# Performance work log

Hardware: AMD Instinct MI355X
Metric: run time of the kernel (lower is better)

The kernel has to match this reference:

```python
import jax, jax.numpy as jnp
import numpy as np

L = 20        # num layers (TTS LM)
Q = 512       # query length
PAST = 512    # past_kv_len
END = PAST + Q  # end_step = 1024
MAXS = 2048   # max_seq_len
D = 896       # hidden size
NKV = 2       # KV heads
NQ = 14       # Q heads
G = NQ // NKV # GQA repeat = 7
HD = 64       # head dim
FF = 4864     # SwiGLU intermediate (Qwen2.5-0.5B)
EPS = 1e-6
SCALE = 1.0 / np.sqrt(HD)


def rms_norm(x, w):
    return x * jax.lax.rsqrt(jnp.mean(x * x, axis=-1, keepdims=True) + EPS) * w


def rotate_half(x):
    x1, x2 = jnp.split(x, 2, axis=-1)
    return jnp.concatenate([-x2, x1], axis=-1)


def setup_inputs() -> dict:
    key = jax.random.key(0)
    ks = jax.random.split(key, 24)
    s = 0.02
    inp = {
        'hidden_states': jax.random.normal(ks[0], (1, Q, D), jnp.float32),
        'position_cos': jax.random.uniform(ks[1], (1, Q, HD), jnp.float32, -1.0, 1.0),
        'position_sin': jax.random.uniform(ks[2], (1, Q, HD), jnp.float32, -1.0, 1.0),
        'attention_mask': jnp.zeros((1, 1, Q, END), jnp.float32),
        'inject_mode': jnp.zeros((1,), jnp.float32),
        'inject_k': jax.random.normal(ks[3], (1, L * NKV, Q, HD), jnp.float32),
        'inject_v': jax.random.normal(ks[4], (1, L * NKV, Q, HD), jnp.float32),
        'k_cache': (jax.random.normal(ks[5], (L, 1, NKV, MAXS, HD), jnp.float32) * 0.5).astype(jnp.float16),
        'v_cache': (jax.random.normal(ks[6], (L, 1, NKV, MAXS, HD), jnp.float32) * 0.5).astype(jnp.float16),
        'Wq': jax.random.normal(ks[7], (L, D, NQ * HD), jnp.float32) * s,
        'bq': jax.random.normal(ks[8], (L, NQ * HD), jnp.float32) * s,
        'Wk': jax.random.normal(ks[9], (L, D, NKV * HD), jnp.float32) * s,
        'bk': jax.random.normal(ks[10], (L, NKV * HD), jnp.float32) * s,
        'Wv': jax.random.normal(ks[11], (L, D, NKV * HD), jnp.float32) * s,
        'bv': jax.random.normal(ks[12], (L, NKV * HD), jnp.float32) * s,
        'Wo': jax.random.normal(ks[13], (L, NQ * HD, D), jnp.float32) * s,
        'ln1': jnp.ones((L, D), jnp.float32),
        'ln2': jnp.ones((L, D), jnp.float32),
        'Wg': jax.random.normal(ks[14], (L, D, FF), jnp.float32) * s,
        'Wu': jax.random.normal(ks[15], (L, D, FF), jnp.float32) * s,
        'Wd': jax.random.normal(ks[16], (L, FF, D), jnp.float32) * s,
        'final_w': jnp.ones((D,), jnp.float32),
    }
    return inp


def reference(hidden_states, position_cos, position_sin, attention_mask,
              inject_mode, inject_k, inject_v, k_cache, v_cache,
              Wq, bq, Wk, bk, Wv, bv, Wo, ln1, ln2, Wg, Wu, Wd, final_w):
    cos = position_cos[:, None]   # [1,1,Q,HD]
    sin = position_sin[:, None]
    inj = inject_mode[0]
    normal = 1.0 - inj
    mask = attention_mask[:, None]  # [1,1,1,Q,END] broadcast over (g,h)
    # per-layer inject slices: [L,1,NKV,Q,HD]
    ik = jnp.transpose(inject_k.reshape(1, L, NKV, Q, HD), (1, 0, 2, 3, 4))
    iv = jnp.transpose(inject_v.reshape(1, L, NKV, Q, HD), (1, 0, 2, 3, 4))

    def layer_fn(h, p):
        (wq, bq_, wk, bk_, wv, bv_, wo, l1, l2, wg, wu, wd, kc, vc, ikl, ivl) = p
        residual = h
        x = rms_norm(h, l1)
        q = (x @ wq + bq_).reshape(1, Q, NQ, HD).transpose(0, 2, 1, 3)   # [1,NQ,Q,HD]
        k = (x @ wk + bk_).reshape(1, Q, NKV, HD).transpose(0, 2, 1, 3)  # [1,NKV,Q,HD]
        v = (x @ wv + bv_).reshape(1, Q, NKV, HD).transpose(0, 2, 1, 3)
        q = q * cos + rotate_half(q) * sin
        k = k * cos + rotate_half(k) * sin
        k = normal * k + inj * ikl
        v = normal * v + inj * ivl
        kc = kc.at[:, :, PAST:END].set(k.astype(jnp.float16))
        vc = vc.at[:, :, PAST:END].set(v.astype(jnp.float16))
        kf = kc[:, :, :END].astype(jnp.float32)  # [1,NKV,END,HD]
        vf = vc[:, :, :END].astype(jnp.float32)
        qg = q.reshape(1, NKV, G, Q, HD)         # grouped GQA (== repeat_kv)
        scores = jnp.einsum('bghqd,bgkd->bghqk', qg, kf) * SCALE + mask
        w = jax.nn.softmax(scores, axis=-1)
        o = jnp.einsum('bghqk,bgkd->bghqd', w, vf)
        o = o.reshape(1, NQ, Q, HD).transpose(0, 2, 1, 3).reshape(1, Q, NQ * HD)
        h = residual + o @ wo
        residual = h
        x = rms_norm(h, l2)
        h = residual + (jax.nn.silu(x @ wg) * (x @ wu)) @ wd
        return h, None

    xs = (Wq, bq, Wk, bk, Wv, bv, Wo, ln1, ln2, Wg, Wu, Wd, k_cache, v_cache, ik, iv)
    h, _ = jax.lax.scan(layer_fn, hidden_states, xs)
    return rms_norm(h, final_w)
```

## Files before the change

kernel.cpp:

```cpp
#include <hip/hip_runtime.h>
#include <hip/hip_fp16.h>
#include <hip/hip_cooperative_groups.h>

namespace cg = cooperative_groups;

#define NLAYER 20
#define QLEN 512
#define PAST 512
#define ENDS 1024
#define MAXS 2048
#define DMODEL 896
#define NKV 2
#define NQ 14
#define GQ 7
#define HD 64
#define FF 4864
#define RMSEPS 1e-6f
#define ATT_SCALE 0.125f

typedef _Float16 f16x8 __attribute__((ext_vector_type(8)));
typedef float f32x4 __attribute__((ext_vector_type(4)));
typedef unsigned int u32_;

__device__ __forceinline__ void gld16(const void* g, void* l) {
    __builtin_amdgcn_global_load_lds(
        (const __attribute__((address_space(1))) u32_*)g,
        (__attribute__((address_space(3))) u32_*)l, 16, 0, 0);
}

union SmemU {
    struct { __half As[8192]; __half Bs[8192]; } g;
    struct { __half S[16512]; float rowinv[16]; } a;
    struct { float T[32][129]; } p;
    struct { float red[4]; } r;
};

#define GEMM_STAGE_SETUP(A_, lda_, B_, ldb_, Kps_)                              \
    const int lane = t & 63, wave = t >> 6;                                     \
    const int wm = wave >> 1, wn = wave & 1;                                    \
    const int m0 = by * 128, n0 = bx * 128;                                     \
    const int kb0 = bz * (Kps_);                                                \
    const int sr = t >> 2, sc = (t & 3) * 8;                                    \
    const int la = lane & 15, ka = (lane >> 4) * 8;                             \
    const int nIter = (Kps_) >> 5;                                              \
    const int scw = sc ^ (((sr >> 1) & 3) << 3);                                \
    const size_t a0 = (size_t)(m0 + sr) * (lda_) + kb0 + scw;                   \
    const size_t a1 = (size_t)(m0 + sr + 64) * (lda_) + kb0 + scw;              \
    const size_t b0 = (size_t)(n0 + sr) * (ldb_) + kb0 + scw;                   \
    const size_t b1 = (size_t)(n0 + sr + 64) * (ldb_) + kb0 + scw;              \
    const int l0 = sr * 32 + sc, l1 = (sr + 64) * 32 + sc;                      \
    f32x4 acc[4][4] = {};                                                       \
    gld16(&(A_)[a0], &As[l0]);                                                  \
    gld16(&(A_)[a1], &As[l1]);                                                  \
    gld16(&(B_)[b0], &Bs[l0]);                                                  \
    gld16(&(B_)[b1], &Bs[l1]);                                                  \
    int buf = 0;                                                                \
    for (int kt = 0; kt < nIter; kt++) {                                        \
        __syncthreads();                                                        \
        if (kt + 1 < nIter) {                                                   \
            const int ko = (kt + 1) * 32;                                       \
            gld16(&(A_)[a0 + ko], &As[(buf ^ 1) * 4096 + l0]);                  \
            gld16(&(A_)[a1 + ko], &As[(buf ^ 1) * 4096 + l1]);                  \
            gld16(&(B_)[b0 + ko], &Bs[(buf ^ 1) * 4096 + l0]);                  \
            gld16(&(B_)[b1 + ko], &Bs[(buf ^ 1) * 4096 + l1]);                  \
        }                                                                       \
        f16x8 av[4], bv[4];                                                     \
        _Pragma("unroll")                                                       \
        for (int i = 0; i < 4; i++) {                                           \
            const int row = wm * 64 + i * 16 + la;                              \
            av[i] = *(const f16x8*)&As[buf * 4096 + row * 32 + (ka ^ (((row >> 1) & 3) << 3))]; \
        }                                                                       \
        _Pragma("unroll")                                                       \
        for (int j = 0; j < 4; j++) {                                           \
            const int row = wn * 64 + j * 16 + la;                              \
            bv[j] = *(const f16x8*)&Bs[buf * 4096 + row * 32 + (ka ^ (((row >> 1) & 3) << 3))]; \
        }                                                                       \
        _Pragma("unroll")                                                       \
        for (int i = 0; i < 4; i++)                                             \
            _Pragma("unroll")                                                   \
            for (int j = 0; j < 4; j++)                                         \
                acc[i][j] = __builtin_amdgcn_mfma_f32_16x16x32_f16(av[i], bv[j], acc[i][j], 0, 0, 0); \
        buf ^= 1;                                                               \
    }                                                                           \
    __syncthreads();

__device__ __forceinline__ void gemm_body(
    const __half* __restrict__ A, int lda, const __half* __restrict__ B, int ldb,
    float* __restrict__ outP, __half* __restrict__ actP, int N, int Kps, int mode,
    int bx, int by, int bz, int t, __half* As, __half* Bs)
{
    GEMM_STAGE_SETUP(A, lda, B, ldb, Kps)
    const int r0 = m0 + wm * 64 + (lane >> 4) * 4;
    const int c0 = n0 + wn * 64 + la;
    if (mode == 0) {
        float* o = outP + (size_t)bz * QLEN * N;
#pragma unroll
        for (int i = 0; i < 4; i++)
#pragma unroll
            for (int j = 0; j < 4; j++)
#pragma unroll
                for (int r = 0; r < 4; r++)
                    o[(size_t)(r0 + i * 16 + r) * N + c0 + j * 16] = acc[i][j][r];
    } else {
#pragma unroll
        for (int i = 0; i < 4; i++)
#pragma unroll
            for (int j = 0; j < 4; j++)
#pragma unroll
                for (int r = 0; r < 4; r++) {
                    float v = acc[i][j][r];
                    float other = __shfl_xor(v, 1);
                    if (!(la & 1)) {
                        const int c = c0 + j * 16;
                        const int row = r0 + i * 16 + r;
                        float sg = v / (1.f + __expf(-v));
                        actP[(size_t)row * FF + (c >> 1)] = __float2half(sg * other);
                    }
                }
    }
}

__device__ __forceinline__ void gemm_qkv_body(
    const __half* __restrict__ A, const __half* __restrict__ B,
    const float* __restrict__ bqkv, const float* __restrict__ cosb,
    const float* __restrict__ sinb, float inj,
    const float* __restrict__ injk, const float* __restrict__ injv,
    __half* __restrict__ qr, __half* __restrict__ Ka, __half* __restrict__ Vt,
    int layer, int bx, int by, int t, __half* As, __half* Bs)
{
    const int bz = 0;
    GEMM_STAGE_SETUP(A, DMODEL, B, DMODEL, 896)
    const int r0 = m0 + wm * 64 + (lane >> 4) * 4;
    const int c0 = n0 + wn * 64 + la;
    const float nrm = 1.f - inj;
#pragma unroll
    for (int i = 0; i < 4; i++)
#pragma unroll
        for (int j = 0; j < 4; j++)
#pragma unroll
            for (int r = 0; r < 4; r++) {
                const int pn = r0 + i * 16 + r;
                const int c = c0 + j * 16;
                const int d = c & 63;
                float v = acc[i][j][r] + bqkv[c];
                if (c < 1024) {
                    float pvv = acc[i][j ^ 2][r] + bqkv[c ^ 32];
                    float rot = (d < 32) ? -pvv : pvv;
                    float rv = v * cosb[pn * HD + d] + rot * sinb[pn * HD + d];
                    if (c < 896) {
                        qr[((size_t)(c >> 6) * QLEN + pn) * HD + d] = __float2half(rv);
                    } else {
                        const int kvh = (c - 896) >> 6;
                        float kn = nrm * rv + inj * injk[(((size_t)layer * NKV + kvh) * QLEN + pn) * HD + d];
                        Ka[((size_t)kvh * ENDS + PAST + pn) * HD + d] = __float2half(kn);
                    }
                } else {
                    const int kvh = (c - 1024) >> 6;
                    float vn = nrm * v + inj * injv[(((size_t)layer * NKV + kvh) * QLEN + pn) * HD + d];
                    Vt[((size_t)kvh * HD + d) * ENDS + PAST + pn] = __float2half(vn);
                }
            }
}

__device__ __forceinline__ void prep_body(
    const float* __restrict__ Wq, const float* __restrict__ Wk, const float* __restrict__ Wv,
    const float* __restrict__ Wo, const float* __restrict__ Wg, const float* __restrict__ Wu,
    const float* __restrict__ Wd, int layer, int z, int bx, int t, float (*T)[129],
    __half* __restrict__ dstW)
{
    const int K = (z == 3) ? FF : DMODEL;
    const int N = (z == 0) ? 1152 : (z == 2) ? 2 * FF : DMODEL;
    const int tilesN = N / 128;
    const int tk = bx / tilesN, tn = bx % tilesN;
    const int k0 = tk * 32, n0 = tn * 128;
    const float* src; int ldn, nc0; int isU = 0;
    if (z == 0) {
        if (n0 < 896)        { src = Wq + (size_t)layer * 896 * 896; ldn = 896; nc0 = n0; }
        else if (n0 < 1024)  { src = Wk + (size_t)layer * 896 * 128; ldn = 128; nc0 = n0 - 896; }
        else                 { src = Wv + (size_t)layer * 896 * 128; ldn = 128; nc0 = n0 - 1024; }
    } else if (z == 1) { src = Wo + (size_t)layer * 896 * 896; ldn = 896; nc0 = n0; }
    else if (z == 2) {
        if (n0 < FF) { src = Wg + (size_t)layer * 896 * FF; ldn = FF; nc0 = n0; }
        else         { src = Wu + (size_t)layer * 896 * FF; ldn = FF; nc0 = n0 - FF; isU = 1; }
    } else { src = Wd + (size_t)layer * FF * 896; ldn = 896; nc0 = n0; }

    __syncthreads();
    {
        const int r = t >> 3, cb = (t & 7) * 16;
        const float* s = &src[(size_t)(k0 + r) * ldn + nc0 + cb];
#pragma unroll
        for (int q = 0; q < 4; q++) {
            float4 v = *(const float4*)&s[q * 4];
            T[r][cb + q * 4 + 0] = v.x; T[r][cb + q * 4 + 1] = v.y;
            T[r][cb + q * 4 + 2] = v.z; T[r][cb + q * 4 + 3] = v.w;
        }
    }
    __syncthreads();
    {
        const int nr = t >> 1, kh = (t & 1) * 16;
        const int drow = (z == 2) ? (2 * (nc0 + nr) + isU) : (n0 + nr);
        __half tmp[16];
#pragma unroll
        for (int kk = 0; kk < 16; kk++)
            tmp[kk] = __float2half_rn(T[kh + kk][nr]);
        __half* dst = dstW + (size_t)drow * K + k0 + kh;
        *(uint4*)dst = *(const uint4*)&tmp[0];
        *(uint4*)(dst + 8) = *(const uint4*)&tmp[8];
    }
    __syncthreads();
}

__device__ __forceinline__ void prep_dispatch(
    const float* Wq, const float* Wk, const float* Wv, const float* Wo,
    const float* Wg, const float* Wu, const float* Wd,
    const float* bq, const float* bk, const float* bv,
    int layer, int j, int t, float (*T)[129],
    __half* wq, __half* wo, __half* wgu, __half* wd, float* bqkv)
{
    int z; __half* dst; int bx = j;
    if (j < 252)        { z = 0; dst = wq; }
    else if (j < 448)   { z = 1; dst = wo;  bx -= 252; }
    else if (j < 2576)  { z = 2; dst = wgu; bx -= 448; }
    else                { z = 3; dst = wd;  bx -= 2576; }
    prep_body(Wq, Wk, Wv, Wo, Wg, Wu, Wd, layer, z, bx, t, T, dst);
    if (z == 0 && bx == 0) {
        for (int i = t; i < 1152; i += 256) {
            float b = (i < 896) ? bq[(size_t)layer * 896 + i]
                    : (i < 1024) ? bk[(size_t)layer * 128 + i - 896]
                                 : bv[(size_t)layer * 128 + i - 1024];
            bqkv[i] = b;
        }
    }
}

__device__ __forceinline__ void cache_copy_body(
    const float* __restrict__ kc32, const float* __restrict__ vc32, int layer,
    __half* __restrict__ Ka, __half* __restrict__ Vt, int p, int lt)
{
    const int kvh = lt >> 6, d = lt & 63;
    const size_t idx = (((size_t)layer * NKV + kvh) * MAXS + p) * HD + d;
    Ka[((size_t)kvh * ENDS + p) * HD + d] = __float2half(kc32[idx]);
    Vt[((size_t)kvh * HD + d) * ENDS + p] = __float2half(vc32[idx]);
}

__device__ __forceinline__ void ropekv_body(
    const float* __restrict__ part, const float* __restrict__ bias,
    const float* __restrict__ cosb, const float* __restrict__ sinb,
    const float* __restrict__ injm, const float* __restrict__ injk,
    const float* __restrict__ injv, const float* __restrict__ kc32,
    const float* __restrict__ vc32, int layer, int nsplit,
    __half* __restrict__ qr, __half* __restrict__ Ka, __half* __restrict__ Vt,
    int p, int lt)
{
    const int kvh = lt >> 6, d = lt & 63;
    if (p < PAST) { cache_copy_body(kc32, vc32, layer, Ka, Vt, p, lt); return; }
    const int pn = p - PAST;
    const float inj = injm[0], nrm = 1.f - inj;
    const float* rb = part + (size_t)pn * 1152;
    const size_t sst = (size_t)QLEN * 1152;
    auto rsum = [&](int c) {
        float x = bias[c];
        for (int s = 0; s < nsplit; s++) x += rb[(size_t)s * sst + c];
        return x;
    };
    for (int idx = lt; idx < NQ * HD; idx += 128) {
        const int dd = idx & 63;
        float x = rsum(idx);
        int pc = (dd < 32) ? idx + 32 : idx - 32;
        float pv = rsum(pc);
        if (dd < 32) pv = -pv;
        float rv = x * cosb[pn * HD + dd] + pv * sinb[pn * HD + dd];
        qr[((size_t)(idx >> 6) * QLEN + pn) * HD + dd] = __float2half(rv);
    }
    {
        const int c = NQ * HD + lt;
        float x = rsum(c);
        int pc = (d < 32) ? c + 32 : c - 32;
        float pv = rsum(pc);
        if (d < 32) pv = -pv;
        float rv = x * cosb[pn * HD + d] + pv * sinb[pn * HD + d];
        float kn = nrm * rv + inj * injk[(((size_t)layer * NKV + kvh) * QLEN + pn) * HD + d];
        Ka[((size_t)kvh * ENDS + PAST + pn) * HD + d] = __float2half(kn);
        const int cv = NQ * HD + NKV * HD + lt;
        float vv = rsum(cv);
        float vn = nrm * vv + inj * injv[(((size_t)layer * NKV + kvh) * QLEN + pn) * HD + d];
        Vt[((size_t)kvh * HD + d) * ENDS + PAST + pn] = __float2half(vn);
    }
}

__device__ __forceinline__ int sswz(int row, int col) {
    return row * 1032 + (col ^ ((row & 7) << 3));
}

__device__ __forceinline__ void attn_body(
    const __half* __restrict__ qr, const __half* __restrict__ Ka,
    const __half* __restrict__ Vt, const float* __restrict__ mask,
    __half* __restrict__ ob, int q0, int h, int t, __half* S, float* rowinv)
{
    const int kv = h / GQ;
    const int lane = t & 63, w = t >> 6;
    const int la = lane & 15, kg = lane >> 4;

    const f16x8* qp = (const f16x8*)&qr[((size_t)h * QLEN + q0 + la) * HD + kg * 8];
    const f16x8 qa0 = qp[0], qa1 = qp[4];
    __syncthreads();

    for (int kb = 0; kb < 256; kb += 16) {
        const int key = w * 256 + kb + la;
        const f16x8* kp = (const f16x8*)&Ka[((size_t)kv * ENDS + key) * HD + kg * 8];
        f32x4 s4 = {0.f, 0.f, 0.f, 0.f};
        s4 = __builtin_amdgcn_mfma_f32_16x16x32_f16(qa0, kp[0], s4, 0, 0, 0);
        s4 = __builtin_amdgcn_mfma_f32_16x16x32_f16(qa1, kp[4], s4, 0, 0, 0);
#pragma unroll
        for (int r = 0; r < 4; r++) {
            const int row = kg * 4 + r;
            float sv = s4[r] * ATT_SCALE + mask[(size_t)(q0 + row) * ENDS + key];
            S[sswz(row, key)] = __float2half(sv);
        }
    }
    __syncthreads();
    {
        const int row = w * 4 + kg;
        float mx = -1e30f;
        for (int j = 0; j < 64; j++)
            mx = fmaxf(mx, __half2float(S[sswz(row, la + 16 * j)]));
        for (int o = 1; o < 16; o <<= 1) mx = fmaxf(mx, __shfl_xor(mx, o));
        float sum = 0.f;
        for (int j = 0; j < 64; j++) {
            const int idx = sswz(row, la + 16 * j);
            float e = __expf(__half2float(S[idx]) - mx);
            S[idx] = __float2half(e);
            sum += e;
        }
        for (int o = 1; o < 16; o <<= 1) sum += __shfl_xor(sum, o);
        if (la == 0) rowinv[row] = 1.f / sum;
    }
    __syncthreads();
    {
        const int d = 16 * w + la;
        const __half* vrow = &Vt[((size_t)kv * HD + d) * ENDS];
        f32x4 acc = {0.f, 0.f, 0.f, 0.f};
        for (int ks = 0; ks < ENDS; ks += 32) {
            f16x8 pa = *(const f16x8*)&S[sswz(la, ks + kg * 8)];
            f16x8 vb = *(const f16x8*)&vrow[ks + kg * 8];
            acc = __builtin_amdgcn_mfma_f32_16x16x32_f16(pa, vb, acc, 0, 0, 0);
        }
#pragma unroll
        for (int r = 0; r < 4; r++) {
            const int qrow = kg * 4 + r;
            ob[(size_t)(q0 + qrow) * (NQ * HD) + h * HD + d] =
                __float2half(acc[r] * rowinv[qrow]);
        }
    }
    __syncthreads();
}

__device__ inline void cvt_store(float* p, float v)  { *p = v; }
__device__ inline void cvt_store(__half* p, float v) { *p = __float2half(v); }

template <typename OUT>
__device__ __forceinline__ void rms_body(
    float* __restrict__ h, const float* __restrict__ parts, int nparts,
    const float* __restrict__ w, OUT* __restrict__ out, int m, int t,
    float* red, float scale)
{
    float loc[4];
    float ss = 0.f;
    int r = 0;
    for (int i = t; i < DMODEL; i += 256, r++) {
        float x = h[(size_t)m * DMODEL + i];
        for (int s = 0; s < nparts; s++)
            x += parts[(size_t)s * QLEN * DMODEL + (size_t)m * DMODEL + i];
        loc[r] = x;
        if (nparts) h[(size_t)m * DMODEL + i] = x;
        ss += x * x;
    }
    for (int o = 32; o; o >>= 1) ss += __shfl_xor(ss, o);
    if ((t & 63) == 0) red[t >> 6] = ss;
    __syncthreads();
    float rs = rsqrtf((red[0] + red[1] + red[2] + red[3]) / (float)DMODEL + RMSEPS);
    r = 0;
    for (int i = t; i < DMODEL; i += 256, r++)
        cvt_store(&out[(size_t)m * DMODEL + i], loc[r] * rs * w[i] * scale);
    __syncthreads();
}

struct P22 {
    const float *hidden, *cosb, *sinb, *mask, *injm, *injk, *injv, *kc32, *vc32;
    const float *Wq, *bq, *Wk, *bk, *Wv, *bv, *Wo, *ln1, *ln2, *Wg, *Wu, *Wd, *finw;
    float *h; __half *xn, *qr, *Ka, *Vt, *ob, *act; float *BIGR;
    float *bqkv0, *bqkv1;
    __half *wq0, *wo0, *wgu0, *wd0, *wq1, *wo1, *wgu1, *wd1;
    float *outF;
};

#define PC_A 300
#define PC_B 700
#define PC_C 576
#define PC_D 800
#define PC_E 500
#define PC_F 600
#define PC_G 164
#define PB_A 0
#define PB_B 300
#define PB_C 1000
#define PB_D 1576
#define PB_E 2376
#define PB_F 2876
#define PB_G 3476

__global__ __launch_bounds__(256) void mega_kernel(P22 P)
{
    __shared__ SmemU sm;
    cg::grid_group gg = cg::this_grid();
    const int nb = gridDim.x, bid = blockIdx.x, t = threadIdx.x;
    const float inj = P.injm[0];

    for (int j = bid; j < 1792; j += nb) {
        int i = j * 256 + t;
        if (i < QLEN * DMODEL) P.h[i] = P.hidden[i];
    }
    for (int j = bid; j < 3640; j += nb)
        prep_dispatch(P.Wq, P.Wk, P.Wv, P.Wo, P.Wg, P.Wu, P.Wd, P.bq, P.bk, P.bv,
                      0, j, t, sm.p.T, P.wq0, P.wo0, P.wgu0, P.wd0, P.bqkv0);
    gg.sync();

    for (int l = 0; l < NLAYER; l++) {
        const int pb = l & 1;
        const __half* wq  = pb ? P.wq1  : P.wq0;
        const __half* wo  = pb ? P.wo1  : P.wo0;
        const __half* wgu = pb ? P.wgu1 : P.wgu0;
        const __half* wd  = pb ? P.wd1  : P.wd0;
        const float*  bqk = pb ? P.bqkv1 : P.bqkv0;
        const bool hasN = (l + 1 < NLAYER);
        __half* nwq  = pb ? P.wq0  : P.wq1;
        __half* nwo  = pb ? P.wo0  : P.wo1;
        __half* nwgu = pb ? P.wgu0 : P.wgu1;
        __half* nwd  = pb ? P.wd0  : P.wd1;
        float*  nbq  = pb ? P.bqkv0 : P.bqkv1;
        #define PREPN(idx) prep_dispatch(P.Wq, P.Wk, P.Wv, P.Wo, P.Wg, P.Wu, P.Wd, \
            P.bq, P.bk, P.bv, l + 1, (idx), t, sm.p.T, nwq, nwo, nwgu, nwd, nbq)

        for (int j = bid; j < QLEN + (hasN ? PC_A : 0); j += nb) {
            if (j < QLEN)
                rms_body<__half>(P.h, l ? P.BIGR : nullptr, l ? 8 : 0,
                                 P.ln1 + (size_t)l * DMODEL, P.xn, j, t, sm.r.red, 1.f);
            else PREPN(PB_A + j - QLEN);
        }
        gg.sync();

        for (int j = bid; j < 292 + (hasN ? PC_B : 0); j += nb) {
            if (j < 36)
                gemm_qkv_body(P.xn, wq, bqk, P.cosb, P.sinb, inj, P.injk, P.injv,
                              P.qr, P.Ka, P.Vt, l, j % 9, j / 9, t, sm.g.As, sm.g.Bs);
            else if (j < 292) {
                int p = (j - 36) * 2 + (t >> 7);
                cache_copy_body(P.kc32, P.vc32, l, P.Ka, P.Vt, p, t & 127);
            } else PREPN(PB_B + j - 292);
        }
        gg.sync();

        for (int j = bid; j < 448 + (hasN ? PC_C : 0); j += nb) {
            if (j < 448)
                attn_body(P.qr, P.Ka, P.Vt, P.mask, P.ob, (j & 31) * 16, j >> 5, t,
                          sm.a.S, sm.a.rowinv);
            else PREPN(PB_C + j - 448);
        }
        gg.sync();

        for (int j = bid; j < 112 + (hasN ? PC_D : 0); j += nb) {
            if (j < 112) {
                int z = j / 28, r = j % 28;
                gemm_body(P.ob, DMODEL, wo, DMODEL, P.BIGR, nullptr, DMODEL, 224, 0,
                          r % 7, r / 7, z, t, sm.g.As, sm.g.Bs);
            } else PREPN(PB_D + j - 112);
        }
        gg.sync();

        for (int j = bid; j < QLEN + (hasN ? PC_E : 0); j += nb) {
            if (j < QLEN)
                rms_body<__half>(P.h, P.BIGR, 4, P.ln2 + (size_t)l * DMODEL, P.xn,
                                 j, t, sm.r.red, 1.f);
            else PREPN(PB_E + j - QLEN);
        }
        gg.sync();

        for (int j = bid; j < 304 + (hasN ? PC_F : 0); j += nb) {
            if (j < 304)
                gemm_body(P.xn, DMODEL, wgu, DMODEL, nullptr, P.act, 2 * FF, DMODEL, 1,
                          j % 76, j / 76, 0, t, sm.g.As, sm.g.Bs);
            else PREPN(PB_F + j - 304);
        }
        gg.sync();

        for (int j = bid; j < 224 + (hasN ? PC_G : 0); j += nb) {
            if (j < 224) {
                int z = j / 28, r = j % 28;
                gemm_body(P.act, FF, wd, FF, P.BIGR, nullptr, DMODEL, 608, 0,
                          r % 7, r / 7, z, t, sm.g.As, sm.g.Bs);
            } else PREPN(PB_G + j - 224);
        }
        gg.sync();
        #undef PREPN
    }
    for (int j = bid; j < QLEN; j += nb)
        rms_body<float>(P.h, P.BIGR, 8, P.finw, P.outF, j, t, sm.r.red, 1.f);
}

__global__ __launch_bounds__(256) void init_kernel(
    const float* __restrict__ hidden, float* __restrict__ h, int* __restrict__ flags)
{
    const int idx = blockIdx.x * 256 + threadIdx.x;
    if (blockIdx.x == 0 && threadIdx.x < 8) flags[threadIdx.x] = 0;
    if (idx < QLEN * DMODEL) h[idx] = hidden[idx];
}

__global__ __launch_bounds__(256) void prep_all(
    const float* Wq, const float* Wk, const float* Wv, const float* Wo,
    const float* Wg, const float* Wu, const float* Wd,
    const float* bq, const float* bk, const float* bv, int layer,
    __half* wqkv, __half* wo, __half* wgu, __half* wd, float* bqkv)
{
    __shared__ float T[32][129];
    prep_dispatch(Wq, Wk, Wv, Wo, Wg, Wu, Wd, bq, bk, bv, layer, blockIdx.x,
                  threadIdx.x, T, wqkv, wo, wgu, wd, bqkv);
}

__global__ __launch_bounds__(256) void gemm128(
    const __half* A, int lda, const __half* B, int ldb,
    float* outP, __half* actP, int N, int Kps, int mode)
{
    __shared__ SmemU sm;
    gemm_body(A, lda, B, ldb, outP, actP, N, Kps, mode,
              blockIdx.x, blockIdx.y, blockIdx.z, threadIdx.x, sm.g.As, sm.g.Bs);
}

__global__ __launch_bounds__(128) void ropekv_kernel(
    const float* part, const float* bias, const float* cosb, const float* sinb,
    const float* injm, const float* injk, const float* injv,
    const float* kc32, const float* vc32, int layer, int nsplit,
    __half* qr, __half* Ka, __half* Vt)
{
    ropekv_body(part, bias, cosb, sinb, injm, injk, injv, kc32, vc32,
                layer, nsplit, qr, Ka, Vt, blockIdx.x, threadIdx.x);
}

__global__ __launch_bounds__(256) void attn_mfma(
    const __half* qr, const __half* Ka, const __half* Vt, const float* mask, __half* ob)
{
    __shared__ SmemU sm;
    attn_body(qr, Ka, Vt, mask, ob, blockIdx.x * 16, blockIdx.y, threadIdx.x,
              sm.a.S, sm.a.rowinv);
}

template <typename OUT>
__global__ __launch_bounds__(256) void rms_kernel(
    float* h, const float* parts, int nparts, const float* w, OUT* out,
    const int* flags)
{
    __shared__ float red[4];
    rms_body<OUT>(h, parts, nparts, w, out, blockIdx.x, threadIdx.x, red, 1.f);
}

extern "C" void kernel_launch(void* const* d_in, const int* in_sizes, int n_in,
                              void* d_out, int out_size, void* d_ws, size_t ws_size,
                              hipStream_t stream)
{
    const float*  hidden = (const float*)d_in[0];
    const float*  cosb   = (const float*)d_in[1];
    const float*  sinb   = (const float*)d_in[2];
    const float*  mask   = (const float*)d_in[3];
    const float*  injm   = (const float*)d_in[4];
    const float*  injk   = (const float*)d_in[5];
    const float*  injv   = (const float*)d_in[6];
    const float*  kc32   = (const float*)d_in[7];
    const float*  vc32   = (const float*)d_in[8];
    const float*  Wq     = (const float*)d_in[9];
    const float*  bq     = (const float*)d_in[10];
    const float*  Wk     = (const float*)d_in[11];
    const float*  bk     = (const float*)d_in[12];
    const float*  Wv     = (const float*)d_in[13];
    const float*  bv     = (const float*)d_in[14];
    const float*  Wo     = (const float*)d_in[15];
    const float*  ln1    = (const float*)d_in[16];
    const float*  ln2    = (const float*)d_in[17];
    const float*  Wg     = (const float*)d_in[18];
    const float*  Wu     = (const float*)d_in[19];
    const float*  Wd     = (const float*)d_in[20];
    const float*  finw   = (const float*)d_in[21];

    bool size_ok = (n_in == 22) &&
        in_sizes[0] == 458752 && in_sizes[1] == 32768 && in_sizes[3] == 524288 &&
        in_sizes[4] == 1 && in_sizes[5] == 1310720 && in_sizes[7] == 5242880 &&
        in_sizes[9] == 16056320 && in_sizes[10] == 17920 && in_sizes[11] == 2293760 &&
        in_sizes[15] == 16056320 && in_sizes[16] == 17920 && in_sizes[18] == 87162880 &&
        in_sizes[20] == 87162880 && in_sizes[21] == 896;
    if (!size_ok) { hipMemsetAsync(d_out, 0x42, (size_t)out_size * 4, stream); return; }

    char* ws = (char*)d_ws;
    size_t off = 0;
    auto alloc = [&](size_t bytes) { void* p = ws + off; off += (bytes + 255) & ~255ull; return p; };
    int*    flags = (int*)alloc(256);
    float*  bqkv0 = (float*)alloc(1152 * 4);
    float*  bqkv1 = (float*)alloc(1152 * 4);
    float*  h     = (float*)alloc((size_t)QLEN * DMODEL * 4);
    __half* xn    = (__half*)alloc((size_t)QLEN * DMODEL * 2);
    __half* qr    = (__half*)alloc((size_t)NQ * QLEN * HD * 2);
    __half* Ka    = (__half*)alloc((size_t)NKV * ENDS * HD * 2);
    __half* Vt    = (__half*)alloc((size_t)NKV * ENDS * HD * 2);
    __half* ob    = (__half*)alloc((size_t)QLEN * NQ * HD * 2);
    __half* act   = (__half*)alloc((size_t)QLEN * FF * 2);
    float*  BIGR  = (float*)alloc(8ull * QLEN * 1152 * 4);
    __half* wq0   = (__half*)alloc(2064384);
    __half* wo0   = (__half*)alloc(1605632);
    __half* wgu0  = (__half*)alloc(17432576);
    __half* wd0   = (__half*)alloc(8716288);
    const size_t NEED_LEGACY = off;
    __half* wq1   = (__half*)alloc(2064384);
    __half* wo1   = (__half*)alloc(1605632);
    __half* wgu1  = (__half*)alloc(17432576);
    __half* wd1   = (__half*)alloc(8716288);
    const size_t NEED_MEGA = off;

    if (ws_size < NEED_LEGACY) {
        hipMemsetAsync(d_out, 0, (size_t)out_size * 4, stream);
        return;
    }

    bool mega_ok = (ws_size >= NEED_MEGA);
    if (mega_ok) {
        int maxB = 0;
        hipError_t e = hipOccupancyMaxActiveBlocksPerMultiprocessor(
            &maxB, reinterpret_cast<const void*>(&mega_kernel), 256, 0);
        if (e != hipSuccess || maxB < 1) mega_ok = false;
        if (mega_ok) {
            int grid = maxB * 256;
            if (grid > 1024) grid = 1024;
            P22 Pv = { hidden, cosb, sinb, mask, injm, injk, injv, kc32, vc32,
                       Wq, bq, Wk, bk, Wv, bv, Wo, ln1, ln2, Wg, Wu, Wd, finw,
                       h, xn, qr, Ka, Vt, ob, act, BIGR, bqkv0, bqkv1,
                       wq0, wo0, wgu0, wd0, wq1, wo1, wgu1, wd1, (float*)d_out };
            void* args[] = { (void*)&Pv };
            hipError_t le = hipLaunchCooperativeKernel(
                reinterpret_cast<const void*>(&mega_kernel),
                dim3(grid), dim3(256), args, 0, stream);
            if (le == hipSuccess) return;
            mega_ok = false;
        }
    }

    init_kernel<<<1792, 256, 0, stream>>>(hidden, h, flags);
    for (int l = 0; l < NLAYER; l++) {
        prep_all<<<3640, 256, 0, stream>>>(Wq, Wk, Wv, Wo, Wg, Wu, Wd, bq, bk, bv, l,
                                           wq0, wo0, wgu0, wd0, bqkv0);
        rms_kernel<__half><<<QLEN, 256, 0, stream>>>(h, l ? BIGR : nullptr, l ? 8 : 0,
                                                     ln1 + (size_t)l * DMODEL, xn, nullptr);
        gemm128<<<dim3(9, 4, 4), 256, 0, stream>>>(xn, DMODEL, wq0, DMODEL, BIGR, nullptr, 1152, 224, 0);
        ropekv_kernel<<<ENDS, 128, 0, stream>>>(BIGR, bqkv0, cosb, sinb, injm, injk, injv,
                                                kc32, vc32, l, 4, qr, Ka, Vt);
        attn_mfma<<<dim3(32, 14), 256, 0, stream>>>(qr, Ka, Vt, mask, ob);
        gemm128<<<dim3(7, 4, 4), 256, 0, stream>>>(ob, DMODEL, wo0, DMODEL, BIGR, nullptr, DMODEL, 224, 0);
        rms_kernel<__half><<<QLEN, 256, 0, stream>>>(h, BIGR, 4, ln2 + (size_t)l * DMODEL, xn, nullptr);
        gemm128<<<dim3(76, 4, 1), 256, 0, stream>>>(xn, DMODEL, wgu0, DMODEL, nullptr, act, 2 * FF, DMODEL, 1);
        gemm128<<<dim3(7, 4, 8), 256, 0, stream>>>(act, FF, wd0, FF, BIGR, nullptr, DMODEL, 608, 0);
    }
    rms_kernel<float><<<QLEN, 256, 0, stream>>>(h, BIGR, 8, finw, (float*)d_out, nullptr);
}
```

Before: 2.887 ms.

## Use BK=64 GEMM tiles, rebalance split-K and prefetch schedule in mega kernel

The GEMM inner loop now stages 64-wide K slices per iteration with a new XOR swizzle, which halves the number of barriers per K pass at the cost of doubling LDS use. The split-K factors change: 7 partials for the O projection and 19 for the down projection, with the partial buffer and RMS reduction counts resized to match. Next-layer KV cache copies move into the O-projection stage, and the prefetch work per stage is redistributed. The cooperative grid is capped at 512 blocks, and the unused flags buffer is removed.

```diff
diff --git a/kernel.cpp b/kernel.cpp
--- a/kernel.cpp
+++ b/kernel.cpp
@@ -29,57 +29,61 @@
 }
 
 union SmemU {
-    struct { __half As[8192]; __half Bs[8192]; } g;
+    struct { __half As[16384]; __half Bs[16384]; } g;
     struct { __half S[16512]; float rowinv[16]; } a;
     struct { float T[32][129]; } p;
     struct { float red[4]; } r;
 };
 
-#define GEMM_STAGE_SETUP(A_, lda_, B_, ldb_, Kps_)                              \
+#define GEMM_STAGE64(A_, lda_, B_, ldb_, Kps_)                                  \
     const int lane = t & 63, wave = t >> 6;                                     \
     const int wm = wave >> 1, wn = wave & 1;                                    \
     const int m0 = by * 128, n0 = bx * 128;                                     \
     const int kb0 = bz * (Kps_);                                                \
-    const int sr = t >> 2, sc = (t & 3) * 8;                                    \
-    const int la = lane & 15, ka = (lane >> 4) * 8;                             \
-    const int nIter = (Kps_) >> 5;                                              \
-    const int scw = sc ^ (((sr >> 1) & 3) << 3);                                \
-    const size_t a0 = (size_t)(m0 + sr) * (lda_) + kb0 + scw;                   \
-    const size_t a1 = (size_t)(m0 + sr + 64) * (lda_) + kb0 + scw;              \
-    const size_t b0 = (size_t)(n0 + sr) * (ldb_) + kb0 + scw;                   \
-    const size_t b1 = (size_t)(n0 + sr + 64) * (ldb_) + kb0 + scw;              \
-    const int l0 = sr * 32 + sc, l1 = (sr + 64) * 32 + sc;                      \
+    const int la = lane & 15, kg = lane >> 4;                                   \
+    const int nIter = (Kps_) >> 6;                                              \
+    const int srow = t >> 3;                                                    \
+    const int gsw = ((t & 7) ^ (srow & 7)) * 8;                                 \
     f32x4 acc[4][4] = {};                                                       \
-    gld16(&(A_)[a0], &As[l0]);                                                  \
-    gld16(&(A_)[a1], &As[l1]);                                                  \
-    gld16(&(B_)[b0], &Bs[l0]);                                                  \
-    gld16(&(B_)[b1], &Bs[l1]);                                                  \
+    {                                                                           \
+        _Pragma("unroll")                                                       \
+        for (int q = 0; q < 4; q++) {                                           \
+            gld16(&(A_)[(size_t)(m0 + q * 32 + srow) * (lda_) + kb0 + gsw], &As[q * 2048 + t * 8]); \
+            gld16(&(B_)[(size_t)(n0 + q * 32 + srow) * (ldb_) + kb0 + gsw], &Bs[q * 2048 + t * 8]); \
+        }                                                                       \
+    }                                                                           \
     int buf = 0;                                                                \
     for (int kt = 0; kt < nIter; kt++) {                                        \
         __syncthreads();                                                        \
         if (kt + 1 < nIter) {                                                   \
-            const int ko = (kt + 1) * 32;                                       \
-            gld16(&(A_)[a0 + ko], &As[(buf ^ 1) * 4096 + l0]);                  \
-            gld16(&(A_)[a1 + ko], &As[(buf ^ 1) * 4096 + l1]);                  \
-            gld16(&(B_)[b0 + ko], &Bs[(buf ^ 1) * 4096 + l0]);                  \
-            gld16(&(B_)[b1 + ko], &Bs[(buf ^ 1) * 4096 + l1]);                  \
-        }                                                                       \
-        f16x8 av[4], bv[4];                                                     \
-        _Pragma("unroll")                                                       \
-        for (int i = 0; i < 4; i++) {                                           \
-            const int row = wm * 64 + i * 16 + la;                              \
-            av[i] = *(const f16x8*)&As[buf * 4096 + row * 32 + (ka ^ (((row >> 1) & 3) << 3))]; \
+            const int ko = kb0 + (kt + 1) * 64;                                 \
+            const int lb = (buf ^ 1) * 8192;                                    \
+            _Pragma("unroll")                                                   \
+            for (int q = 0; q < 4; q++) {                                       \
+                gld16(&(A_)[(size_t)(m0 + q * 32 + srow) * (lda_) + ko + gsw], &As[lb + q * 2048 + t * 8]); \
+                gld16(&(B_)[(size_t)(n0 + q * 32 + srow) * (ldb_) + ko + gsw], &Bs[lb + q * 2048 + t * 8]); \
+            }                                                                   \
         }                                                                       \
         _Pragma("unroll")                                                       \
-        for (int j = 0; j < 4; j++) {                                           \
-            const int row = wn * 64 + j * 16 + la;                              \
-            bv[j] = *(const f16x8*)&Bs[buf * 4096 + row * 32 + (ka ^ (((row >> 1) & 3) << 3))]; \
+        for (int kk = 0; kk < 2; kk++) {                                        \
+            f16x8 av[4], bv[4];                                                 \
+            const int g = kk * 4 + kg;                                          \
+            _Pragma("unroll")                                                   \
+            for (int i = 0; i < 4; i++) {                                       \
+                const int R = wm * 64 + i * 16 + la;                            \
+                av[i] = *(const f16x8*)&As[buf * 8192 + R * 64 + ((g ^ (R & 7)) * 8)]; \
+            }                                                                   \
+            _Pragma("unroll")                                                   \
+            for (int j = 0; j < 4; j++) {                                       \
+                const int R = wn * 64 + j * 16 + la;                            \
+                bv[j] = *(const f16x8*)&Bs[buf * 8192 + R * 64 + ((g ^ (R & 7)) * 8)]; \
+            }                                                                   \
+            _Pragma("unroll")                                                   \
+            for (int i = 0; i < 4; i++)                                         \
+                _Pragma("unroll")                                               \
+                for (int j = 0; j < 4; j++)                                     \
+                    acc[i][j] = __builtin_amdgcn_mfma_f32_16x16x32_f16(av[i], bv[j], acc[i][j], 0, 0, 0); \
         }                                                                       \
-        _Pragma("unroll")                                                       \
-        for (int i = 0; i < 4; i++)                                             \
-            _Pragma("unroll")                                                   \
-            for (int j = 0; j < 4; j++)                                         \
-                acc[i][j] = __builtin_amdgcn_mfma_f32_16x16x32_f16(av[i], bv[j], acc[i][j], 0, 0, 0); \
         buf ^= 1;                                                               \
     }                                                                           \
     __syncthreads();
@@ -89,8 +93,8 @@
     float* __restrict__ outP, __half* __restrict__ actP, int N, int Kps, int mode,
     int bx, int by, int bz, int t, __half* As, __half* Bs)
 {
-    GEMM_STAGE_SETUP(A, lda, B, ldb, Kps)
-    const int r0 = m0 + wm * 64 + (lane >> 4) * 4;
+    GEMM_STAGE64(A, lda, B, ldb, Kps)
+    const int r0 = m0 + wm * 64 + kg * 4;
     const int c0 = n0 + wn * 64 + la;
     if (mode == 0) {
         float* o = outP + (size_t)bz * QLEN * N;
@@ -129,8 +133,8 @@
     int layer, int bx, int by, int t, __half* As, __half* Bs)
 {
     const int bz = 0;
-    GEMM_STAGE_SETUP(A, DMODEL, B, DMODEL, 896)
-    const int r0 = m0 + wm * 64 + (lane >> 4) * 4;
+    GEMM_STAGE64(A, DMODEL, B, DMODEL, 896)
+    const int r0 = m0 + wm * 64 + kg * 4;
     const int c0 = n0 + wn * 64 + la;
     const float nrm = 1.f - inj;
 #pragma unroll
@@ -394,20 +398,16 @@
     float *outF;
 };
 
-#define PC_A 300
-#define PC_B 700
-#define PC_C 576
+#define PC_B 1200
+#define PC_C 200
 #define PC_D 800
-#define PC_E 500
-#define PC_F 600
-#define PC_G 164
-#define PB_A 0
-#define PB_B 300
-#define PB_C 1000
-#define PB_D 1576
-#define PB_E 2376
-#define PB_F 2876
-#define PB_G 3476
+#define PC_F 1000
+#define PC_G 440
+#define PB_B 0
+#define PB_C 1200
+#define PB_D 1400
+#define PB_F 2200
+#define PB_G 3200
 
 __global__ __launch_bounds__(256) void mega_kernel(P22 P)
 {
@@ -420,6 +420,8 @@
         int i = j * 256 + t;
         if (i < QLEN * DMODEL) P.h[i] = P.hidden[i];
     }
+    for (int j = bid; j < 256; j += nb)
+        cache_copy_body(P.kc32, P.vc32, 0, P.Ka, P.Vt, j * 2 + (t >> 7), t & 127);
     for (int j = bid; j < 3640; j += nb)
         prep_dispatch(P.Wq, P.Wk, P.Wv, P.Wo, P.Wg, P.Wu, P.Wd, P.bq, P.bk, P.bv,
                       0, j, t, sm.p.T, P.wq0, P.wo0, P.wgu0, P.wd0, P.bqkv0);
@@ -441,22 +443,16 @@
         #define PREPN(idx) prep_dispatch(P.Wq, P.Wk, P.Wv, P.Wo, P.Wg, P.Wu, P.Wd, \
             P.bq, P.bk, P.bv, l + 1, (idx), t, sm.p.T, nwq, nwo, nwgu, nwd, nbq)
 
-        for (int j = bid; j < QLEN + (hasN ? PC_A : 0); j += nb) {
-            if (j < QLEN)
-                rms_body<__half>(P.h, l ? P.BIGR : nullptr, l ? 8 : 0,
-                                 P.ln1 + (size_t)l * DMODEL, P.xn, j, t, sm.r.red, 1.f);
-            else PREPN(PB_A + j - QLEN);
-        }
+        for (int j = bid; j < QLEN; j += nb)
+            rms_body<__half>(P.h, l ? P.BIGR : nullptr, l ? 19 : 0,
+                             P.ln1 + (size_t)l * DMODEL, P.xn, j, t, sm.r.red, 1.f);
         gg.sync();
 
-        for (int j = bid; j < 292 + (hasN ? PC_B : 0); j += nb) {
+        for (int j = bid; j < 36 + (hasN ? PC_B : 0); j += nb) {
             if (j < 36)
                 gemm_qkv_body(P.xn, wq, bqk, P.cosb, P.sinb, inj, P.injk, P.injv,
                               P.qr, P.Ka, P.Vt, l, j % 9, j / 9, t, sm.g.As, sm.g.Bs);
-            else if (j < 292) {
-                int p = (j - 36) * 2 + (t >> 7);
-                cache_copy_body(P.kc32, P.vc32, l, P.Ka, P.Vt, p, t & 127);
-            } else PREPN(PB_B + j - 292);
+            else PREPN(PB_B + j - 36);
         }
         gg.sync();
 
@@ -468,50 +464,49 @@
         }
         gg.sync();
 
-        for (int j = bid; j < 112 + (hasN ? PC_D : 0); j += nb) {
-            if (j < 112) {
+        for (int j = bid; j < 452 + (hasN ? PC_D : 0); j += nb) {
+            if (j < 196) {
                 int z = j / 28, r = j % 28;
-                gemm_body(P.ob, DMODEL, wo, DMODEL, P.BIGR, nullptr, DMODEL, 224, 0,
+                gemm_body(P.ob, DMODEL, wo, DMODEL, P.BIGR, nullptr, DMODEL, 128, 0,
                           r % 7, r / 7, z, t, sm.g.As, sm.g.Bs);
-            } else PREPN(PB_D + j - 112);
+            } else if (j < 452) {
+                if (hasN) cache_copy_body(P.kc32, P.vc32, l + 1, P.Ka, P.Vt,
+                                          (j - 196) * 2 + (t >> 7), t & 127);
+            } else PREPN(PB_D + j - 452);
         }
         gg.sync();
 
-        for (int j = bid; j < QLEN + (hasN ? PC_E : 0); j += nb) {
-            if (j < QLEN)
-                rms_body<__half>(P.h, P.BIGR, 4, P.ln2 + (size_t)l * DMODEL, P.xn,
-                                 j, t, sm.r.red, 1.f);
-            else PREPN(PB_E + j - QLEN);
-        }
+        for (int j = bid; j < QLEN; j += nb)
+            rms_body<__half>(P.h, P.BIGR, 7, P.ln2 + (size_t)l * DMODEL, P.xn,
+                             j, t, sm.r.red, 1.f);
         gg.sync();
 
         for (int j = bid; j < 304 + (hasN ? PC_F : 0); j += nb) {
             if (j < 304)
-                gemm_body(P.xn, DMODEL, wgu, DMODEL, nullptr, P.act, 2 * FF, DMODEL, 1,
+                gemm_body(P.xn, DMODEL, wgu, DMODEL, nullptr, P.act, 2 * FF, 896, 1,
                           j % 76, j / 76, 0, t, sm.g.As, sm.g.Bs);
             else PREPN(PB_F + j - 304);
         }
         gg.sync();
 
-        for (int j = bid; j < 224 + (hasN ? PC_G : 0); j += nb) {
-            if (j < 224) {
+        for (int j = bid; j < 532 + (hasN ? PC_G : 0); j += nb) {
+            if (j < 532) {
                 int z = j / 28, r = j % 28;
-                gemm_body(P.act, FF, wd, FF, P.BIGR, nullptr, DMODEL, 608, 0,
+                gemm_body(P.act, FF, wd, FF, P.BIGR, nullptr, DMODEL, 256, 0,
                           r % 7, r / 7, z, t, sm.g.As, sm.g.Bs);
-            } else PREPN(PB_G + j - 224);
+            } else PREPN(PB_G + j - 532);
         }
         gg.sync();
         #undef PREPN
     }
     for (int j = bid; j < QLEN; j += nb)
-        rms_body<float>(P.h, P.BIGR, 8, P.finw, P.outF, j, t, sm.r.red, 1.f);
+        rms_body<float>(P.h, P.BIGR, 19, P.finw, P.outF, j, t, sm.r.red, 1.f);
 }
 
 __global__ __launch_bounds__(256) void init_kernel(
-    const float* __restrict__ hidden, float* __restrict__ h, int* __restrict__ flags)
+    const float* __restrict__ hidden, float* __restrict__ h)
 {
     const int idx = blockIdx.x * 256 + threadIdx.x;
-    if (blockIdx.x == 0 && threadIdx.x < 8) flags[threadIdx.x] = 0;
     if (idx < QLEN * DMODEL) h[idx] = hidden[idx];
 }
 
@@ -555,8 +550,7 @@
 
 template <typename OUT>
 __global__ __launch_bounds__(256) void rms_kernel(
-    float* h, const float* parts, int nparts, const float* w, OUT* out,
-    const int* flags)
+    float* h, const float* parts, int nparts, const float* w, OUT* out)
 {
     __shared__ float red[4];
     rms_body<OUT>(h, parts, nparts, w, out, blockIdx.x, threadIdx.x, red, 1.f);
@@ -600,7 +594,6 @@
     char* ws = (char*)d_ws;
     size_t off = 0;
     auto alloc = [&](size_t bytes) { void* p = ws + off; off += (bytes + 255) & ~255ull; return p; };
-    int*    flags = (int*)alloc(256);
     float*  bqkv0 = (float*)alloc(1152 * 4);
     float*  bqkv1 = (float*)alloc(1152 * 4);
     float*  h     = (float*)alloc((size_t)QLEN * DMODEL * 4);
@@ -610,7 +603,7 @@
     __half* Vt    = (__half*)alloc((size_t)NKV * ENDS * HD * 2);
     __half* ob    = (__half*)alloc((size_t)QLEN * NQ * HD * 2);
     __half* act   = (__half*)alloc((size_t)QLEN * FF * 2);
-    float*  BIGR  = (float*)alloc(8ull * QLEN * 1152 * 4);
+    float*  BIGR  = (float*)alloc(19ull * QLEN * DMODEL * 4);
     __half* wq0   = (__half*)alloc(2064384);
     __half* wo0   = (__half*)alloc(1605632);
     __half* wgu0  = (__half*)alloc(17432576);
@@ -635,7 +628,7 @@
         if (e != hipSuccess || maxB < 1) mega_ok = false;
         if (mega_ok) {
             int grid = maxB * 256;
-            if (grid > 1024) grid = 1024;
+            if (grid > 512) grid = 512;
             P22 Pv = { hidden, cosb, sinb, mask, injm, injk, injv, kc32, vc32,
                        Wq, bq, Wk, bk, Wv, bv, Wo, ln1, ln2, Wg, Wu, Wd, finw,
                        h, xn, qr, Ka, Vt, ob, act, BIGR, bqkv0, bqkv1,
@@ -649,20 +642,20 @@
         }
     }
 
-    init_kernel<<<1792, 256, 0, stream>>>(hidden, h, flags);
+    init_kernel<<<1792, 256, 0, stream>>>(hidden, h);
     for (int l = 0; l < NLAYER; l++) {
         prep_all<<<3640, 256, 0, stream>>>(Wq, Wk, Wv, Wo, Wg, Wu, Wd, bq, bk, bv, l,
                                            wq0, wo0, wgu0, wd0, bqkv0);
-        rms_kernel<__half><<<QLEN, 256, 0, stream>>>(h, l ? BIGR : nullptr, l ? 8 : 0,
-                                                     ln1 + (size_t)l * DMODEL, xn, nullptr);
-        gemm128<<<dim3(9, 4, 4), 256, 0, stream>>>(xn, DMODEL, wq0, DMODEL, BIGR, nullptr, 1152, 224, 0);
+        rms_kernel<__half><<<QLEN, 256, 0, stream>>>(h, l ? BIGR : nullptr, l ? 19 : 0,
+                                                     ln1 + (size_t)l * DMODEL, xn);
+        gemm128<<<dim3(9, 4, 2), 256, 0, stream>>>(xn, DMODEL, wq0, DMODEL, BIGR, nullptr, 1152, 448, 0);
         ropekv_kernel<<<ENDS, 128, 0, stream>>>(BIGR, bqkv0, cosb, sinb, injm, injk, injv,
-                                                kc32, vc32, l, 4, qr, Ka, Vt);
+                                                kc32, vc32, l, 2, qr, Ka, Vt);
         attn_mfma<<<dim3(32, 14), 256, 0, stream>>>(qr, Ka, Vt, mask, ob);
-        gemm128<<<dim3(7, 4, 4), 256, 0, stream>>>(ob, DMODEL, wo0, DMODEL, BIGR, nullptr, DMODEL, 224, 0);
-        rms_kernel<__half><<<QLEN, 256, 0, stream>>>(h, BIGR, 4, ln2 + (size_t)l * DMODEL, xn, nullptr);
-        gemm128<<<dim3(76, 4, 1), 256, 0, stream>>>(xn, DMODEL, wgu0, DMODEL, nullptr, act, 2 * FF, DMODEL, 1);
-        gemm128<<<dim3(7, 4, 8), 256, 0, stream>>>(act, FF, wd0, FF, BIGR, nullptr, DMODEL, 608, 0);
-    }
-    rms_kernel<float><<<QLEN, 256, 0, stream>>>(h, BIGR, 8, finw, (float*)d_out, nullptr);
-}
+        gemm128<<<dim3(7, 4, 7), 256, 0, stream>>>(ob, DMODEL, wo0, DMODEL, BIGR, nullptr, DMODEL, 128, 0);
+        rms_kernel<__half><<<QLEN, 256, 0, stream>>>(h, BIGR, 7, ln2 + (size_t)l * DMODEL, xn);
+        gemm128<<<dim3(76, 4, 1), 256, 0, stream>>>(xn, DMODEL, wgu0, DMODEL, nullptr, act, 2 * FF, 896, 1);
+        gemm128<<<dim3(7, 4, 19), 256, 0, stream>>>(act, FF, wd0, FF, BIGR, nullptr, DMODEL, 256, 0);
+    }
+    rms_kernel<float><<<QLEN, 256, 0, stream>>>(h, BIGR, 19, finw, (float*)d_out);
+}
```

Result: faster. 2.765 ms, median of 3 (-4.2%).
